# Optimization experiments

Measured on AMD Instinct MI355X. Metric: run time of the kernel, lower is better.

Reference implementation:

```python
import jax, jax.numpy as jnp
import numpy as np

N_NODES = 100000
E_RAW = 1600000
SKIP_COEFF = 0.5
NEG_SLOPE = 0.2
BN_EPS = 1e-5


def _gat_conv(x, src, dst, W, a_src, a_dst, b, heads, out_ch):
    # PyG GATConv (concat=True). x: [N, F_in], W: [F_in, heads*out_ch]
    N = x.shape[0]
    h = (x @ W).reshape(N, heads, out_ch)                      # [N,H,C]
    alpha_src = jnp.sum(h * a_src, axis=-1)                    # [N,H]
    alpha_dst = jnp.sum(h * a_dst, axis=-1)                    # [N,H]
    e = jax.nn.leaky_relu(alpha_src[src] + alpha_dst[dst], NEG_SLOPE)  # [E,H]
    # segment softmax over incoming edges of each destination node
    m = jax.ops.segment_max(e, dst, num_segments=N)            # [N,H]
    p = jnp.exp(e - m[dst])
    denom = jax.ops.segment_sum(p, dst, num_segments=N)        # [N,H]
    alpha = p / denom[dst]                                      # [E,H]
    out = jax.ops.segment_sum(h[src] * alpha[:, :, None], dst, num_segments=N)
    return out.reshape(N, heads * out_ch) + b


def _bn(x, gamma, beta):
    # BatchNorm1d, training-mode batch statistics (biased variance)
    mu = jnp.mean(x, axis=0)
    var = jnp.var(x, axis=0)
    return (x - mu) * jax.lax.rsqrt(var + BN_EPS) * gamma + beta


def _glorot(key, shape):
    fan = shape[0] + shape[-1] if len(shape) == 2 else shape[-1] * 2
    s = jnp.sqrt(6.0 / fan)
    return jax.random.uniform(key, shape, jnp.float32, -s, s)


def setup_inputs() -> dict:
    key = jax.random.key(0)
    ks = jax.random.split(key, 24)
    x = jax.random.normal(ks[0], (N_NODES, 128), jnp.float32)
    edge_index = jax.random.randint(ks[1], (2, E_RAW), 0, N_NODES, jnp.int64)
    d = {"x": x, "edge_index": edge_index}
    # conv0: 128 -> (4 heads x 32); conv1,conv2: 128 -> (4x32); conv3: 128 -> (1x64)
    dims = [(128, 4, 32), (128, 4, 32), (128, 4, 32), (128, 1, 64)]
    ki = 2
    for l, (fin, H, C) in enumerate(dims):
        d[f"W{l}"] = _glorot(ks[ki], (fin, H * C)); ki += 1
        d[f"as{l}"] = _glorot(ks[ki], (H, C)); ki += 1
        d[f"ad{l}"] = _glorot(ks[ki], (H, C)); ki += 1
        d[f"b{l}"] = jnp.zeros((H * C,), jnp.float32)
    d["g1"] = jnp.ones((128,), jnp.float32)
    d["be1"] = jnp.zeros((128,), jnp.float32)
    d["g2"] = jnp.ones((128,), jnp.float32)
    d["be2"] = jnp.zeros((128,), jnp.float32)
    return d


def reference(x, edge_index, W0, as0, ad0, b0, W1, as1, ad1, b1,
              W2, as2, ad2, b2, W3, as3, ad3, b3, g1, be1, g2, be2):
    N = x.shape[0]
    loops = jnp.arange(N, dtype=edge_index.dtype)
    src = jnp.concatenate([edge_index[0], loops])  # add self-loops (PyG default)
    dst = jnp.concatenate([edge_index[1], loops])

    h = _gat_conv(x, src, dst, W0, as0, ad0, b0, 4, 32)        # [N,128]
    h_skip = h
    # i = 1
    h = _gat_conv(h, src, dst, W1, as1, ad1, b1, 4, 32)
    h = jax.nn.relu(_bn(h, g1, be1))
    out1 = h
    # i = 2 (skip branch)
    h = _gat_conv(h, src, dst, W2, as2, ad2, b2, 4, 32)
    h = _bn(h, g2, be2) + SKIP_COEFF * h_skip
    h = jax.nn.relu(h)
    out2 = h

    h = out1 + out2
    return _gat_conv(h, src, dst, W3, as3, ad3, b3, 1, 64)      # [N,64]
```

## Files before the change

### kernel.cpp

```cpp
#include <hip/hip_runtime.h>
#include <cstdint>
#include <cstddef>


typedef unsigned int uint;
typedef unsigned short ushort_t;
typedef __attribute__((ext_vector_type(8))) short bf16x8_t;
typedef __attribute__((ext_vector_type(4))) float f32x4_t;

__device__ __forceinline__ float leaky(float e) { return e < 0.f ? 0.2f * e : e; }
__device__ __forceinline__ float bflo(uint u) { return __uint_as_float(u << 16); }
__device__ __forceinline__ float bfhi(uint u) { return __uint_as_float(u & 0xffff0000u); }
__device__ __forceinline__ ushort_t f2bf(float f) {
  uint u = __float_as_uint(f);
  u += 0x7fffu + ((u >> 16) & 1u);
  return (ushort_t)(u >> 16);
}
__device__ __forceinline__ float bf2f(ushort_t h) { return __uint_as_float((uint)h << 16); }
__device__ __forceinline__ uint pack2(float a, float b) {
  return (uint)f2bf(a) | ((uint)f2bf(b) << 16);
}


__global__ __launch_bounds__(256) void k_deg(const int* __restrict__ ei, int ER, int ET,
                                             int* __restrict__ deg) {
  int e = blockIdx.x * 256 + threadIdx.x;
  if (e >= ET) return;
  int d = (e < ER) ? ei[ER + e] : (e - ER);
  atomicAdd(&deg[d], 1);
}

__global__ __launch_bounds__(256) void k_scan1(const int* __restrict__ deg, int* __restrict__ rp,
                                               int* __restrict__ bsums, int n) {
  __shared__ int sh[256];
  int tid = threadIdx.x;
  int base = blockIdx.x * 2048 + tid * 8;
  int pre[8];
  int s = 0;
#pragma unroll
  for (int j = 0; j < 8; ++j) {
    int idx = base + j;
    int v = (idx < n) ? deg[idx] : 0;
    pre[j] = s;
    s += v;
  }
  sh[tid] = s;
  __syncthreads();
  for (int d = 1; d < 256; d <<= 1) {
    int t = (tid >= d) ? sh[tid - d] : 0;
    __syncthreads();
    if (tid >= d) sh[tid] += t;
    __syncthreads();
  }
  int excl = sh[tid] - s;
#pragma unroll
  for (int j = 0; j < 8; ++j) {
    int idx = base + j;
    if (idx < n) rp[idx] = excl + pre[j];
  }
  if (tid == 255) bsums[blockIdx.x] = sh[255];
}

__global__ void k_scan2(int* bsums, int nb) {
  for (int i = 1; i < nb; ++i) bsums[i] += bsums[i - 1];
}

__global__ __launch_bounds__(256) void k_scan3(int* __restrict__ rp, const int* __restrict__ bsums,
                                               int n, int ET) {
  int i = blockIdx.x * 256 + threadIdx.x;
  if (i > n) return;
  if (i == n) { rp[n] = ET; return; }
  int b = i >> 11;
  if (b > 0) rp[i] += bsums[b - 1];
}

__global__ __launch_bounds__(256) void k_scatter(const int* __restrict__ ei, int ER, int ET,
                                                 const int* __restrict__ rp, int* __restrict__ fill,
                                                 int* __restrict__ col) {
  int e = blockIdx.x * 256 + threadIdx.x;
  if (e >= ET) return;
  int s, d;
  if (e < ER) { s = ei[e]; d = ei[ER + e]; } else { s = e - ER; d = s; }
  int pos = rp[d] + atomicAdd(&fill[d], 1);
  col[pos] = s;
}


__global__ __launch_bounds__(256) void k_prepW(const float* __restrict__ W0,
                                               const float* __restrict__ W1,
                                               const float* __restrict__ W2,
                                               const float* __restrict__ W3,
                                               ushort_t* __restrict__ Wthi,
                                               ushort_t* __restrict__ Wtlo) {
  int id = blockIdx.x * 256 + threadIdx.x;
  int l = id >> 14;
  if (l >= 4) return;
  int t = id & 16383;
  int j = t >> 7, k = t & 127;
  const float* W = (l == 0) ? W0 : (l == 1) ? W1 : (l == 2) ? W2 : W3;
  int cols = (l == 3) ? 64 : 128;
  if (j >= cols) return;
  float v = W[(size_t)k * cols + j];
  ushort_t hi = f2bf(v);
  float rem = v - bf2f(hi);
  Wthi[(size_t)l * 16384 + j * 128 + k] = hi;
  Wtlo[(size_t)l * 16384 + j * 128 + k] = f2bf(rem);
}


__global__ __launch_bounds__(256) void k_split(const float* __restrict__ in,
                                               uint* __restrict__ hi2, uint* __restrict__ lo2,
                                               int n4) {
  int i = blockIdx.x * 256 + threadIdx.x;
  if (i >= n4) return;
  float4 v = ((const float4*)in)[i];
  ushort_t hx = f2bf(v.x), hy = f2bf(v.y), hz = f2bf(v.z), hw = f2bf(v.w);
  uint2 h = make_uint2((uint)hx | ((uint)hy << 16), (uint)hz | ((uint)hw << 16));
  uint2 l = make_uint2(pack2(v.x - bf2f(hx), v.y - bf2f(hy)),
                       pack2(v.z - bf2f(hz), v.w - bf2f(hw)));
  ((uint2*)hi2)[i] = h;
  ((uint2*)lo2)[i] = l;
}


template <int COLS, int H>
__global__ __launch_bounds__(256) void k_mm(const ushort_t* __restrict__ Ahi,
                                            const ushort_t* __restrict__ Alo,
                                            const ushort_t* __restrict__ Wthi,
                                            const ushort_t* __restrict__ Wtlo,
                                            const float* __restrict__ aS,
                                            const float* __restrict__ aD,
                                            ushort_t* __restrict__ hbf,
                                            float* __restrict__ asg,
                                            float* __restrict__ adg, int N) {
  constexpr int NB = COLS / 16;
  __shared__ __align__(16) ushort_t sWhi[COLS * 136];
  __shared__ __align__(16) ushort_t sWlo[COLS * 136];
  int tid = threadIdx.x;
  int lane = tid & 63, wv = tid >> 6;
  int lj = lane & 15, lg = lane >> 4;
  int r0 = blockIdx.x * 64 + wv * 16;

  for (int idx = tid; idx < COLS * 16; idx += 256) {
    int j = idx >> 4, seg = idx & 15;
    uint4 vh = *(const uint4*)(Wthi + (size_t)j * 128 + seg * 8);
    uint4 vl = *(const uint4*)(Wtlo + (size_t)j * 128 + seg * 8);
    *(uint4*)&sWhi[j * 136 + seg * 8] = vh;
    *(uint4*)&sWlo[j * 136 + seg * 8] = vl;
  }
  __syncthreads();

  f32x4_t acc[NB];
#pragma unroll
  for (int cb = 0; cb < NB; ++cb) acc[cb] = (f32x4_t){0.f, 0.f, 0.f, 0.f};

  int rowc = r0 + lj; if (rowc >= N) rowc = N - 1;
  const ushort_t* apH = Ahi + (size_t)rowc * 128 + lg * 8;
  const ushort_t* apL = Alo + (size_t)rowc * 128 + lg * 8;

#pragma unroll
  for (int kc = 0; kc < 4; ++kc) {
    bf16x8_t ah = *(const bf16x8_t*)(apH + kc * 32);
    bf16x8_t al = *(const bf16x8_t*)(apL + kc * 32);
#pragma unroll
    for (int cb = 0; cb < NB; ++cb) {
      int boff = (cb * 16 + lj) * 136 + kc * 32 + lg * 8;
      bf16x8_t bh = *(const bf16x8_t*)&sWhi[boff];
      bf16x8_t bl = *(const bf16x8_t*)&sWlo[boff];
      acc[cb] = __builtin_amdgcn_mfma_f32_16x16x32_bf16(ah, bh, acc[cb], 0, 0, 0);
      acc[cb] = __builtin_amdgcn_mfma_f32_16x16x32_bf16(al, bh, acc[cb], 0, 0, 0);
      acc[cb] = __builtin_amdgcn_mfma_f32_16x16x32_bf16(ah, bl, acc[cb], 0, 0, 0);
    }
  }

  float asv[NB], adv[NB];
#pragma unroll
  for (int cb = 0; cb < NB; ++cb) {
    asv[cb] = aS[cb * 16 + lj];
    adv[cb] = aD[cb * 16 + lj];
  }
#pragma unroll
  for (int reg = 0; reg < 4; ++reg) {
    int row = r0 + lg * 4 + reg;
    if (H == 4) {
      float ps[4] = {0.f, 0.f, 0.f, 0.f}, pd[4] = {0.f, 0.f, 0.f, 0.f};
#pragma unroll
      for (int cb = 0; cb < NB; ++cb) {
        int h = cb >> 1;
        ps[h] += acc[cb][reg] * asv[cb];
        pd[h] += acc[cb][reg] * adv[cb];
      }
#pragma unroll
      for (int m = 1; m < 16; m <<= 1) {
#pragma unroll
        for (int h = 0; h < 4; ++h) {
          ps[h] += __shfl_xor(ps[h], m);
          pd[h] += __shfl_xor(pd[h], m);
        }
      }
      if (lj == 0 && row < N) {
        *(float4*)(asg + (size_t)row * 4) = make_float4(ps[0], ps[1], ps[2], ps[3]);
        *(float4*)(adg + (size_t)row * 4) = make_float4(pd[0], pd[1], pd[2], pd[3]);
      }
    } else {
      float ps = 0.f, pd = 0.f;
#pragma unroll
      for (int cb = 0; cb < NB; ++cb) {
        ps += acc[cb][reg] * asv[cb];
        pd += acc[cb][reg] * adv[cb];
      }
#pragma unroll
      for (int m = 1; m < 16; m <<= 1) {
        ps += __shfl_xor(ps, m);
        pd += __shfl_xor(pd, m);
      }
      if (lj == 0 && row < N) { asg[row] = ps; adg[row] = pd; }
    }
  }

  __syncthreads();
  ushort_t* bnc = sWhi + wv * (16 * 136);
#pragma unroll
  for (int cb = 0; cb < NB; ++cb)
#pragma unroll
    for (int reg = 0; reg < 4; ++reg)
      bnc[(lg * 4 + reg) * 136 + cb * 16 + lj] = f2bf(acc[cb][reg]);
  constexpr int UPR = COLS / 8;
  constexpr int NPASS = 16 * UPR / 64;
#pragma unroll
  for (int p = 0; p < NPASS; ++p) {
    int u = p * 64 + lane;
    int rl = u / UPR, sg = u % UPR;
    if (r0 + rl < N)
      *(uint4*)(hbf + (size_t)(r0 + rl) * COLS + sg * 8) = *(const uint4*)&bnc[rl * 136 + sg * 8];
  }
}


template <int H, int C, int MODE>
__global__ __launch_bounds__(256) void k_agg(const int* __restrict__ rp, const int* __restrict__ col,
                                             const ushort_t* __restrict__ hbf,
                                             const float* __restrict__ asg,
                                             const float* __restrict__ adg,
                                             const float* __restrict__ bias,
                                             float* __restrict__ out,
                                             uint* __restrict__ outp,
                                             uint* __restrict__ ohi, uint* __restrict__ olo,
                                             int N) {
  constexpr int HC = H * C;
  __shared__ float shp[4][64 * H];
  int lane = threadIdx.x & 63;
  int wv = threadIdx.x >> 6;
  int n = blockIdx.x * 4 + wv;
  if (n >= N) return;
  int hd = (H == 4) ? (lane >> 4) : 0;

  float d0 = 0.f, d1 = 0.f, d2 = 0.f, d3 = 0.f;
  if (H == 4) {
    float4 t = *(const float4*)(adg + (size_t)n * 4);
    d0 = t.x; d1 = t.y; d2 = t.z; d3 = t.w;
  } else {
    d0 = adg[n];
  }

  int s0 = rp[n], s1 = rp[n + 1];
  float denom = 0.f, a0 = 0.f, a1 = 0.f;

  for (int base = s0; base < s1; base += 64) {
    int lim = s1 - base; if (lim > 64) lim = 64;
    int j = base + lane;
    bool valid = j < s1;
    int cj = valid ? col[j] : 0;

    if (H == 4) {
      float4 t = *(const float4*)(asg + (size_t)cj * 4);
      float4 p;
      p.x = valid ? __expf(leaky(t.x + d0)) : 0.f;
      p.y = valid ? __expf(leaky(t.y + d1)) : 0.f;
      p.z = valid ? __expf(leaky(t.z + d2)) : 0.f;
      p.w = valid ? __expf(leaky(t.w + d3)) : 0.f;
      *(float4*)&shp[wv][lane * 4] = p;
    } else {
      float t = asg[cj];
      shp[wv][lane] = valid ? __expf(leaky(t + d0)) : 0.f;
    }
    __builtin_amdgcn_sched_barrier(0);

    for (int i = 0; i < lim; ++i) {
      int s = __shfl(cj, i);
      float p = (H == 4) ? shp[wv][i * 4 + hd] : shp[wv][i];
      if (H == 4) {
        uint hv = *(const uint*)(hbf + (size_t)s * HC + lane * 2);
        a0 += p * bflo(hv);
        a1 += p * bfhi(hv);
      } else {
        uint hv = (uint)hbf[(size_t)s * HC + lane];
        a0 += p * __uint_as_float(hv << 16);
      }
      denom += p;
    }
  }

  float inv = 1.f / denom;
  if (H == 4) {
    float o0 = a0 * inv + bias[lane * 2];
    float o1 = a1 * inv + bias[lane * 2 + 1];
    if (MODE == 0) {
      *(float2*)(out + (size_t)n * HC + lane * 2) = make_float2(o0, o1);
    } else {
      ushort_t hx = f2bf(o0), hy = f2bf(o1);
      uint hw = (uint)hx | ((uint)hy << 16);
      outp[(size_t)n * 64 + lane] = hw;
      ohi[(size_t)n * 64 + lane] = hw;
      olo[(size_t)n * 64 + lane] = pack2(o0 - bf2f(hx), o1 - bf2f(hy));
    }
  } else {
    out[(size_t)n * HC + lane] = a0 * inv + bias[lane];
  }
}


__global__ __launch_bounds__(512) void k_bnstats1(const float* __restrict__ t,
                                                  float* __restrict__ p1, float* __restrict__ p2,
                                                  int N) {
  __shared__ float ls[4][128], ls2[4][128];
  int c = threadIdx.x & 127, q = threadIdx.x >> 7;
  float s = 0.f, s2 = 0.f;
  for (int r = blockIdx.x * 4 + q; r < N; r += gridDim.x * 4) {
    float v = t[(size_t)r * 128 + c];
    s += v;
    s2 += v * v;
  }
  ls[q][c] = s; ls2[q][c] = s2;
  __syncthreads();
  if (q == 0) {
    s = ls[0][c] + ls[1][c] + ls[2][c] + ls[3][c];
    s2 = ls2[0][c] + ls2[1][c] + ls2[2][c] + ls2[3][c];
    p1[blockIdx.x * 128 + c] = s;
    p2[blockIdx.x * 128 + c] = s2;
  }
}

__global__ void k_bnstats2(const float* __restrict__ p1, const float* __restrict__ p2,
                           float* __restrict__ mu, float* __restrict__ rstd, int G, int N) {
  int c = threadIdx.x;
  float s = 0.f, s2 = 0.f;
  for (int b = 0; b < G; ++b) { s += p1[b * 128 + c]; s2 += p2[b * 128 + c]; }
  float m = s / (float)N;
  float var = s2 / (float)N - m * m;
  mu[c] = m;
  rstd[c] = rsqrtf(var + 1e-5f);
}

__global__ __launch_bounds__(256) void k_bnapply1(const float* __restrict__ t,
                                                  const float* __restrict__ mu,
                                                  const float* __restrict__ rstd,
                                                  const float* __restrict__ g,
                                                  const float* __restrict__ be,
                                                  uint* __restrict__ o1p,
                                                  uint* __restrict__ ohi, uint* __restrict__ olo,
                                                  int n4) {
  int i = blockIdx.x * 256 + threadIdx.x;
  if (i >= n4) return;
  float4 v = ((const float4*)t)[i];
  int c = (i & 31) * 4;
  float4 r;
  r.x = fmaxf((v.x - mu[c + 0]) * rstd[c + 0] * g[c + 0] + be[c + 0], 0.f);
  r.y = fmaxf((v.y - mu[c + 1]) * rstd[c + 1] * g[c + 1] + be[c + 1], 0.f);
  r.z = fmaxf((v.z - mu[c + 2]) * rstd[c + 2] * g[c + 2] + be[c + 2], 0.f);
  r.w = fmaxf((v.w - mu[c + 3]) * rstd[c + 3] * g[c + 3] + be[c + 3], 0.f);
  ushort_t hx = f2bf(r.x), hy = f2bf(r.y), hz = f2bf(r.z), hw = f2bf(r.w);
  uint2 h = make_uint2((uint)hx | ((uint)hy << 16), (uint)hz | ((uint)hw << 16));
  ((uint2*)o1p)[i] = h;
  ((uint2*)ohi)[i] = h;
  ((uint2*)olo)[i] = make_uint2(pack2(r.x - bf2f(hx), r.y - bf2f(hy)),
                                pack2(r.z - bf2f(hz), r.w - bf2f(hw)));
}

__global__ __launch_bounds__(256) void k_bnapply2(const float* __restrict__ t,
                                                  const uint* __restrict__ skp,
                                                  const uint* __restrict__ o1p,
                                                  const float* __restrict__ mu,
                                                  const float* __restrict__ rstd,
                                                  const float* __restrict__ g,
                                                  const float* __restrict__ be,
                                                  uint* __restrict__ ohi, uint* __restrict__ olo,
                                                  int n4) {
  int i = blockIdx.x * 256 + threadIdx.x;
  if (i >= n4) return;
  float4 v = ((const float4*)t)[i];
  uint2 sku = ((const uint2*)skp)[i];
  uint2 o1u = ((const uint2*)o1p)[i];
  int c = (i & 31) * 4;
  float4 r;
  r.x = bflo(o1u.x) + fmaxf((v.x - mu[c + 0]) * rstd[c + 0] * g[c + 0] + be[c + 0] + 0.5f * bflo(sku.x), 0.f);
  r.y = bfhi(o1u.x) + fmaxf((v.y - mu[c + 1]) * rstd[c + 1] * g[c + 1] + be[c + 1] + 0.5f * bfhi(sku.x), 0.f);
  r.z = bflo(o1u.y) + fmaxf((v.z - mu[c + 2]) * rstd[c + 2] * g[c + 2] + be[c + 2] + 0.5f * bflo(sku.y), 0.f);
  r.w = bfhi(o1u.y) + fmaxf((v.w - mu[c + 3]) * rstd[c + 3] * g[c + 3] + be[c + 3] + 0.5f * bfhi(sku.y), 0.f);
  ushort_t hx = f2bf(r.x), hy = f2bf(r.y), hz = f2bf(r.z), hw = f2bf(r.w);
  ((uint2*)ohi)[i] = make_uint2((uint)hx | ((uint)hy << 16), (uint)hz | ((uint)hw << 16));
  ((uint2*)olo)[i] = make_uint2(pack2(r.x - bf2f(hx), r.y - bf2f(hy)),
                                pack2(r.z - bf2f(hz), r.w - bf2f(hw)));
}


extern "C" void kernel_launch(void* const* d_in, const int* in_sizes, int n_in,
                              void* d_out, int out_size, void* d_ws, size_t ws_size,
                              hipStream_t stream) {
  const float* x = (const float*)d_in[0];
  const int* ei = (const int*)d_in[1];
  const float* W[4]  = {(const float*)d_in[2], (const float*)d_in[6],
                        (const float*)d_in[10], (const float*)d_in[14]};
  const float* AS[4] = {(const float*)d_in[3], (const float*)d_in[7],
                        (const float*)d_in[11], (const float*)d_in[15]};
  const float* AD[4] = {(const float*)d_in[4], (const float*)d_in[8],
                        (const float*)d_in[12], (const float*)d_in[16]};
  const float* B[4]  = {(const float*)d_in[5], (const float*)d_in[9],
                        (const float*)d_in[13], (const float*)d_in[17]};
  const float* g1 = (const float*)d_in[18];
  const float* be1 = (const float*)d_in[19];
  const float* g2 = (const float*)d_in[20];
  const float* be2 = (const float*)d_in[21];

  const int N = in_sizes[0] / 128;
  const int ER = in_sizes[1] / 2;
  const int ET = ER + N;

  char* ws = (char*)d_ws;
  size_t off = 0;
  auto carve = [&](size_t bytes) {
    size_t o = off;
    off = (off + bytes + 255) & ~(size_t)255;
    return (void*)(ws + o);
  };
  int* rowptr     = (int*)carve((size_t)(N + 1) * 4);
  int* col        = (int*)carve((size_t)ET * 4);
  int* bsums      = (int*)carve(64 * 4);
  float* asg      = (float*)carve((size_t)N * 4 * 4);
  float* adg      = (float*)carve((size_t)N * 4 * 4);
  ushort_t* hbf   = (ushort_t*)carve((size_t)N * 128 * 2);
  ushort_t* ahi   = (ushort_t*)carve((size_t)N * 128 * 2);
  ushort_t* alo   = (ushort_t*)carve((size_t)N * 128 * 2);
  uint* skipb     = (uint*)carve((size_t)N * 64 * 4);
  uint* out1b     = (uint*)carve((size_t)N * 64 * 4);
  float* tbuf     = (float*)carve((size_t)N * 128 * 4);
  ushort_t* Wthi  = (ushort_t*)carve(4 * 16384 * 2);
  ushort_t* Wtlo  = (ushort_t*)carve(4 * 16384 * 2);
  float* p1       = (float*)carve(128 * 128 * 4);
  float* p2       = (float*)carve(128 * 128 * 4);
  float* mu       = (float*)carve(128 * 4);
  float* rstd     = (float*)carve(128 * 4);
  int* fill       = (int*)asg;
  (void)ws_size;

  const int nb = (N + 2047) / 2048;
  const int gE = (ET + 255) / 256;
  const int gN4 = (N + 3) / 4;
  const int gM = (N + 63) / 64;
  const int n4 = N * 32;
  const int gP = (n4 + 255) / 256;

  hipMemsetAsync(fill, 0, (size_t)N * 4, stream);
  k_deg<<<gE, 256, 0, stream>>>(ei, ER, ET, fill);
  k_scan1<<<nb, 256, 0, stream>>>(fill, rowptr, bsums, N);
  k_scan2<<<1, 1, 0, stream>>>(bsums, nb);
  k_scan3<<<(N + 256) / 256, 256, 0, stream>>>(rowptr, bsums, N, ET);
  hipMemsetAsync(fill, 0, (size_t)N * 4, stream);
  k_scatter<<<gE, 256, 0, stream>>>(ei, ER, ET, rowptr, fill, col);
  k_prepW<<<256, 256, 0, stream>>>(W[0], W[1], W[2], W[3], Wthi, Wtlo);
  k_split<<<gP, 256, 0, stream>>>(x, (uint*)ahi, (uint*)alo, n4);

  k_mm<128, 4><<<gM, 256, 0, stream>>>(ahi, alo, Wthi, Wtlo, AS[0], AD[0], hbf, asg, adg, N);
  k_agg<4, 32, 1><<<gN4, 256, 0, stream>>>(rowptr, col, hbf, asg, adg, B[0], nullptr,
                                           skipb, (uint*)ahi, (uint*)alo, N);

  k_mm<128, 4><<<gM, 256, 0, stream>>>(ahi, alo, Wthi + 16384, Wtlo + 16384, AS[1], AD[1],
                                       hbf, asg, adg, N);
  k_agg<4, 32, 0><<<gN4, 256, 0, stream>>>(rowptr, col, hbf, asg, adg, B[1], tbuf,
                                           nullptr, nullptr, nullptr, N);
  k_bnstats1<<<128, 512, 0, stream>>>(tbuf, p1, p2, N);
  k_bnstats2<<<1, 128, 0, stream>>>(p1, p2, mu, rstd, 128, N);
  k_bnapply1<<<gP, 256, 0, stream>>>(tbuf, mu, rstd, g1, be1, out1b, (uint*)ahi, (uint*)alo, n4);

  k_mm<128, 4><<<gM, 256, 0, stream>>>(ahi, alo, Wthi + 2 * 16384, Wtlo + 2 * 16384, AS[2], AD[2],
                                       hbf, asg, adg, N);
  k_agg<4, 32, 0><<<gN4, 256, 0, stream>>>(rowptr, col, hbf, asg, adg, B[2], tbuf,
                                           nullptr, nullptr, nullptr, N);
  k_bnstats1<<<128, 512, 0, stream>>>(tbuf, p1, p2, N);
  k_bnstats2<<<1, 128, 0, stream>>>(p1, p2, mu, rstd, 128, N);
  k_bnapply2<<<gP, 256, 0, stream>>>(tbuf, skipb, out1b, mu, rstd, g2, be2,
                                     (uint*)ahi, (uint*)alo, n4);

  k_mm<64, 1><<<gM, 256, 0, stream>>>(ahi, alo, Wthi + 3 * 16384, Wtlo + 3 * 16384, AS[3], AD[3],
                                      hbf, asg, adg, N);
  k_agg<1, 64, 0><<<gN4, 256, 0, stream>>>(rowptr, col, hbf, asg, adg, B[3], (float*)d_out,
                                           nullptr, nullptr, nullptr, N);
}
```

Measured before the change: 1.097 ms.

## Process several edges per wavefront in GAT aggregation with 16-byte row loads

The aggregation kernel now splits each 64-lane wavefront into groups: each lane loads 8 bf16 features (16 bytes) of a neighbour row, so several edges are gathered at once instead of one edge per loop step. Partial sums and the softmax denominator are then combined with xor-shuffle reductions, and only the first group writes vectorized outputs. This targets the serial, latency-bound per-edge gather loop by raising memory-level parallelism and cutting loop trip counts. It adds an end-of-loop shuffle reduction, more registers per lane, and wasted loads of row 0 for padding edges when the degree is not a multiple of the group count.

```diff
diff --git a/kernel.cpp b/kernel.cpp
--- a/kernel.cpp
+++ b/kernel.cpp
@@ -248,12 +248,18 @@
                                              uint* __restrict__ ohi, uint* __restrict__ olo,
                                              int N) {
   constexpr int HC = H * C;
+  constexpr int LPE = HC / 8;
+  constexpr int EPI = 64 / LPE;
   __shared__ float shp[4][64 * H];
   int lane = threadIdx.x & 63;
   int wv = threadIdx.x >> 6;
   int n = blockIdx.x * 4 + wv;
   if (n >= N) return;
-  int hd = (H == 4) ? (lane >> 4) : 0;
+
+  int sub = lane / LPE;
+  int le = lane % LPE;
+  int ch0 = le * 8;
+  int head = (H == 4) ? (ch0 >> 5) : 0;
 
   float d0 = 0.f, d1 = 0.f, d2 = 0.f, d3 = 0.f;
   if (H == 4) {
@@ -264,7 +270,10 @@
   }
 
   int s0 = rp[n], s1 = rp[n + 1];
-  float denom = 0.f, a0 = 0.f, a1 = 0.f;
+  float denom = 0.f;
+  float a[8];
+#pragma unroll
+  for (int k = 0; k < 8; ++k) a[k] = 0.f;
 
   for (int base = s0; base < s1; base += 64) {
     int lim = s1 - base; if (lim > 64) lim = 64;
@@ -286,36 +295,50 @@
     }
     __builtin_amdgcn_sched_barrier(0);
 
-    for (int i = 0; i < lim; ++i) {
-      int s = __shfl(cj, i);
-      float p = (H == 4) ? shp[wv][i * 4 + hd] : shp[wv][i];
-      if (H == 4) {
-        uint hv = *(const uint*)(hbf + (size_t)s * HC + lane * 2);
-        a0 += p * bflo(hv);
-        a1 += p * bfhi(hv);
-      } else {
-        uint hv = (uint)hbf[(size_t)s * HC + lane];
-        a0 += p * __uint_as_float(hv << 16);
-      }
+    for (int i = 0; i < lim; i += EPI) {
+      int e = i + sub;
+      int s = __shfl(cj, e);
+      float p = (H == 4) ? shp[wv][e * 4 + head] : shp[wv][e];
+      uint4 hv = *(const uint4*)(hbf + (size_t)s * HC + ch0);
+      a[0] += p * bflo(hv.x); a[1] += p * bfhi(hv.x);
+      a[2] += p * bflo(hv.y); a[3] += p * bfhi(hv.y);
+      a[4] += p * bflo(hv.z); a[5] += p * bfhi(hv.z);
+      a[6] += p * bflo(hv.w); a[7] += p * bfhi(hv.w);
       denom += p;
     }
   }
 
+#pragma unroll
+  for (int m = LPE; m < 64; m <<= 1) {
+#pragma unroll
+    for (int k = 0; k < 8; ++k) a[k] += __shfl_xor(a[k], m);
+    denom += __shfl_xor(denom, m);
+  }
+
+  if (sub != 0) return;
   float inv = 1.f / denom;
-  if (H == 4) {
-    float o0 = a0 * inv + bias[lane * 2];
-    float o1 = a1 * inv + bias[lane * 2 + 1];
-    if (MODE == 0) {
-      *(float2*)(out + (size_t)n * HC + lane * 2) = make_float2(o0, o1);
-    } else {
-      ushort_t hx = f2bf(o0), hy = f2bf(o1);
-      uint hw = (uint)hx | ((uint)hy << 16);
-      outp[(size_t)n * 64 + lane] = hw;
-      ohi[(size_t)n * 64 + lane] = hw;
-      olo[(size_t)n * 64 + lane] = pack2(o0 - bf2f(hx), o1 - bf2f(hy));
+  float o[8];
+#pragma unroll
+  for (int k = 0; k < 8; ++k) o[k] = a[k] * inv + bias[ch0 + k];
+
+  if (MODE == 0) {
+    float4 w0 = make_float4(o[0], o[1], o[2], o[3]);
+    float4 w1 = make_float4(o[4], o[5], o[6], o[7]);
+    *(float4*)(out + (size_t)n * HC + ch0) = w0;
+    *(float4*)(out + (size_t)n * HC + ch0 + 4) = w1;
+  } else {
+    uint hw[4], lw[4];
+#pragma unroll
+    for (int k = 0; k < 4; ++k) {
+      ushort_t hx = f2bf(o[2 * k]), hy = f2bf(o[2 * k + 1]);
+      hw[k] = (uint)hx | ((uint)hy << 16);
+      lw[k] = pack2(o[2 * k] - bf2f(hx), o[2 * k + 1] - bf2f(hy));
     }
-  } else {
-    out[(size_t)n * HC + lane] = a0 * inv + bias[lane];
+    uint4 hv = make_uint4(hw[0], hw[1], hw[2], hw[3]);
+    uint4 lv = make_uint4(lw[0], lw[1], lw[2], lw[3]);
+    *(uint4*)(outp + (size_t)n * 64 + le * 4) = hv;
+    *(uint4*)(ohi + (size_t)n * 64 + le * 4) = hv;
+    *(uint4*)(olo + (size_t)n * 64 + le * 4) = lv;
   }
 }
 
```

Result: faster. 916.2 us (-16.5%).
